# Performance work log

Hardware: AMD Instinct MI355X
Metric: run time of the kernel (lower is better)

The kernel has to match this reference:

```python
import jax, jax.numpy as jnp
import numpy as np

B, S, D = 2, 2048, 2048
E, F, TOP_K = 16, 768, 2
NORM_TOPK_PROB = True


def setup_inputs() -> dict:
    key = jax.random.key(0)
    ks = jax.random.split(key, 5)
    sc = 0.02
    return {
        "hidden_states": jax.random.normal(ks[0], (B, S, D), jnp.float32),
        "router_w": jax.random.normal(ks[1], (E, D), jnp.float32) * sc,
        "gate_w": jax.random.normal(ks[2], (E, F, D), jnp.float32) * sc,
        "up_w": jax.random.normal(ks[3], (E, F, D), jnp.float32) * sc,
        "down_w": jax.random.normal(ks[4], (E, D, F), jnp.float32) * sc,
    }


def reference(hidden_states, router_w, gate_w, up_w, down_w):
    b, s, d = hidden_states.shape
    x = hidden_states.reshape(-1, d)                      # [T, D]
    T = x.shape[0]
    # Router: logits, softmax in fp32, top-k
    router_logits = x @ router_w.T                        # [T, E]
    probs = jax.nn.softmax(router_logits.astype(jnp.float32), axis=-1)
    topk_w, topk_idx = jax.lax.top_k(probs, TOP_K)        # [T, K]
    if NORM_TOPK_PROB:
        topk_w = topk_w / jnp.sum(topk_w, axis=-1, keepdims=True)
    topk_w = topk_w.astype(x.dtype)
    # Combine weights as a dense [T, E] matrix (0 for unselected experts);
    # math-equivalent to the per-expert gather/index_add in the original.
    combine = jnp.zeros((T, E), x.dtype).at[jnp.arange(T)[:, None], topk_idx].add(topk_w)
    # Per-expert SwiGLU MLP on all tokens (zero-weight tokens contribute nothing)
    g = jax.nn.silu(jnp.einsum('td,efd->etf', x, gate_w))  # [E, T, F]
    u = jnp.einsum('td,efd->etf', x, up_w)                 # [E, T, F]
    h = (g * u) * combine.T[:, :, None]                    # weight before down-proj
    out = jnp.einsum('etf,edf->td', h, down_w)             # [T, D]
    return out.reshape(b, s, d), router_logits
```

## Files before the change

### kernel.cpp

```cpp
#include <hip/hip_runtime.h>
#include <stdint.h>


#define NTOK 4096
#define DIM  2048
#define NEXP 16
#define FDIM 768
#define BK   32

#define WS_CNT     0
#define WS_CUR     256
#define WS_NTILES  512
#define WS_TILE_E  576
#define WS_TILE_B  736
#define WS_TOKE    1024
#define WS_TOKW    9216
#define WS_SLOTT   17408
#define SLOTW_NEW  27648
#define SLOTW_OLD  26624
#define MAX_TILES  144

#define TMN 128
#define TNA 64
#define TNB 128
#define MAX_SLOTS_N 10240
#define MAX_TILES_N 80
#define TMO 64
#define MAX_SLOTS_O 9216

#define B_XBF  262144ull
#define B_H    (B_XBF + (size_t)NTOK*DIM*2)
#define B_GBF  (B_H + (size_t)MAX_SLOTS_N*FDIM*2)
#define B_UBF  (B_GBF + (size_t)NEXP*FDIM*DIM*2)
#define B_DBF  (B_UBF + (size_t)NEXP*FDIM*DIM*2)
#define WS_NEED (B_DBF + (size_t)NEXP*FDIM*DIM*2)
#define B_HOLD 143360ull

typedef __attribute__((ext_vector_type(8))) short short8;
typedef __attribute__((ext_vector_type(4))) float f32x4;

__device__ __forceinline__ unsigned short f2bf(float f) {
    unsigned u = __float_as_uint(f);
    return (unsigned short)((u + 0x7FFFu + ((u >> 16) & 1u)) >> 16);
}

__device__ __forceinline__ short8 cvt8(float4 v0, float4 v1) {
    short8 s;
    s[0] = (short)f2bf(v0.x); s[1] = (short)f2bf(v0.y);
    s[2] = (short)f2bf(v0.z); s[3] = (short)f2bf(v0.w);
    s[4] = (short)f2bf(v1.x); s[5] = (short)f2bf(v1.y);
    s[6] = (short)f2bf(v1.z); s[7] = (short)f2bf(v1.w);
    return s;
}

__device__ __forceinline__ void gl_lds16(const void* g, void* l) {
    __builtin_amdgcn_global_load_lds(
        (const __attribute__((address_space(1))) unsigned int*)g,
        (__attribute__((address_space(3))) unsigned int*)l, 16, 0, 0);
}

__global__ __launch_bounds__(256) void cvt_k(const float* __restrict__ s,
                                             unsigned short* __restrict__ d, int n8) {
    int i = blockIdx.x * 256 + threadIdx.x;
    if (i < n8) {
        const float4* p = (const float4*)(s + (size_t)i * 8);
        *(short8*)(d + (size_t)i * 8) = cvt8(p[0], p[1]);
    }
}

__global__ __launch_bounds__(256) void router_k(
    const float* __restrict__ x, const float* __restrict__ rw,
    float* __restrict__ logits_out, int* __restrict__ wsi, float* __restrict__ wsf)
{
    int wid = threadIdx.x >> 6, lane = threadIdx.x & 63;
    int t = blockIdx.x * 4 + wid;
    const float* xr = x + (size_t)t * DIM;

    float acc[NEXP];
#pragma unroll
    for (int e = 0; e < NEXP; e++) acc[e] = 0.f;
    for (int i = 0; i < DIM / 64; i++) {
        float xv = xr[i * 64 + lane];
#pragma unroll
        for (int e = 0; e < NEXP; e++) acc[e] += xv * rw[e * DIM + i * 64 + lane];
    }
#pragma unroll
    for (int e = 0; e < NEXP; e++) {
        float v = acc[e];
        for (int off = 32; off; off >>= 1) v += __shfl_down(v, off);
        acc[e] = v;
    }
    if (lane == 0) {
#pragma unroll
        for (int e = 0; e < NEXP; e++) logits_out[t * NEXP + e] = acc[e];
        int i0 = 0; float m0 = acc[0];
#pragma unroll
        for (int e = 1; e < NEXP; e++) if (acc[e] > m0) { m0 = acc[e]; i0 = e; }
        int i1 = -1; float m1 = -3.4e38f;
#pragma unroll
        for (int e = 0; e < NEXP; e++) if (e != i0 && acc[e] > m1) { m1 = acc[e]; i1 = e; }
        float w0 = 1.f / (1.f + __expf(m1 - m0));
        wsi[WS_TOKE + t * 2 + 0] = i0;
        wsi[WS_TOKE + t * 2 + 1] = i1;
        wsf[WS_TOKW + t * 2 + 0] = w0;
        wsf[WS_TOKW + t * 2 + 1] = 1.f - w0;
        atomicAdd(&wsi[WS_CNT + i0 * 16], 1);
        atomicAdd(&wsi[WS_CNT + i1 * 16], 1);
    }
}

__global__ void scan_k(int* __restrict__ wsi, float* __restrict__ wsf,
                       int tm, int slotw, int max_slots)
{
    if (threadIdx.x == 0) {
        int total = 0, tiles = 0;
        for (int e = 0; e < NEXP; e++) {
            int c = wsi[WS_CNT + e * 16];
            int nt = (c + tm - 1) / tm;
            wsi[WS_CNT + e * 16] = total;
            for (int j = 0; j < nt; j++) {
                wsi[WS_TILE_E + tiles] = e;
                wsi[WS_TILE_B + tiles] = total + j * tm;
                tiles++;
            }
            total += nt * tm;
        }
        wsi[WS_NTILES] = tiles;
    }
    for (int s = threadIdx.x; s < max_slots; s += blockDim.x) {
        wsi[WS_SLOTT + s] = 0;
        wsf[slotw + s] = 0.f;
    }
}

__global__ __launch_bounds__(256) void scatter_k(int* __restrict__ wsi,
                                                 float* __restrict__ wsf, int slotw)
{
    int t = blockIdx.x * blockDim.x + threadIdx.x;
    if (t >= NTOK) return;
#pragma unroll
    for (int k = 0; k < 2; k++) {
        int e = wsi[WS_TOKE + t * 2 + k];
        float w = wsf[WS_TOKW + t * 2 + k];
        int pos = atomicAdd(&wsi[WS_CUR + e * 16], 1);
        int s = wsi[WS_CNT + e * 16] + pos;
        wsi[WS_SLOTT + s] = t;
        wsf[slotw + s] = w;
    }
}


__global__ __launch_bounds__(256) void expertA_k(
    const unsigned short* __restrict__ xbf,
    const unsigned short* __restrict__ gbf,
    const unsigned short* __restrict__ ubf,
    const int* __restrict__ wsi, const float* __restrict__ wsf,
    unsigned short* __restrict__ H)
{
    __shared__ unsigned short As[TMN * BK];
    __shared__ unsigned short Gs[TNA * BK];
    __shared__ unsigned short Us[TNA * BK];
    __shared__ unsigned short Hs[TMN][TNA + 8];
    __shared__ int   Ts[TMN];
    __shared__ float Wl[TMN];

    int tile = blockIdx.y;
    if (tile >= wsi[WS_NTILES]) return;
    int e     = wsi[WS_TILE_E + tile];
    int slot0 = wsi[WS_TILE_B + tile];
    int f0    = blockIdx.x * TNA;
    int tid   = threadIdx.x;

    if (tid < TMN) {
        Ts[tid] = wsi[WS_SLOTT + slot0 + tid];
        Wl[tid] = wsf[SLOTW_NEW + slot0 + tid];
    }
    __syncthreads();

    int r0 = tid >> 2, seg = tid & 3;
    const unsigned short* ap0 = xbf + (size_t)Ts[r0] * DIM + seg * 8;
    const unsigned short* ap1 = xbf + (size_t)Ts[64 + r0] * DIM + seg * 8;
    const unsigned short* gp  = gbf + ((size_t)e * FDIM + f0 + r0) * DIM + seg * 8;
    const unsigned short* up  = ubf + ((size_t)e * FDIM + f0 + r0) * DIM + seg * 8;
    unsigned short* lA0 = &As[(size_t)tid * 8];
    unsigned short* lA1 = &As[(size_t)(256 + tid) * 8];
    unsigned short* lG  = &Gs[(size_t)tid * 8];
    unsigned short* lU  = &Us[(size_t)tid * 8];

    int wid = tid >> 6, lane = tid & 63;
    int wm = (wid >> 1) * 64, wn = (wid & 1) * 32;
    int lr = lane & 15, lk = (lane >> 4) * 8;

    f32x4 accg[4][2], accu[4][2];
#pragma unroll
    for (int i = 0; i < 4; i++)
#pragma unroll
        for (int j = 0; j < 2; j++) { accg[i][j] = (f32x4)0.f; accu[i][j] = (f32x4)0.f; }

    for (int k0 = 0; k0 < DIM; k0 += BK) {
        gl_lds16(ap0 + k0, lA0);
        gl_lds16(ap1 + k0, lA1);
        gl_lds16(gp + k0, lG);
        gl_lds16(up + k0, lU);
        __syncthreads();

        short8 a[4], g[2], u[2];
#pragma unroll
        for (int mi = 0; mi < 4; mi++)
            a[mi] = *(const short8*)&As[(wm + mi * 16 + lr) * BK + lk];
#pragma unroll
        for (int nj = 0; nj < 2; nj++) {
            g[nj] = *(const short8*)&Gs[(wn + nj * 16 + lr) * BK + lk];
            u[nj] = *(const short8*)&Us[(wn + nj * 16 + lr) * BK + lk];
        }
#pragma unroll
        for (int mi = 0; mi < 4; mi++)
#pragma unroll
            for (int nj = 0; nj < 2; nj++) {
                accg[mi][nj] = __builtin_amdgcn_mfma_f32_16x16x32_bf16(a[mi], g[nj], accg[mi][nj], 0, 0, 0);
                accu[mi][nj] = __builtin_amdgcn_mfma_f32_16x16x32_bf16(a[mi], u[nj], accu[mi][nj], 0, 0, 0);
            }
        __syncthreads();
    }

#pragma unroll
    for (int mi = 0; mi < 4; mi++)
#pragma unroll
        for (int nj = 0; nj < 2; nj++)
#pragma unroll
            for (int r = 0; r < 4; r++) {
                int m = wm + mi * 16 + (lane >> 4) * 4 + r;
                int n = wn + nj * 16 + lr;
                float g = accg[mi][nj][r];
                float u = accu[mi][nj][r];
                float sg = g / (1.f + __expf(-g));
                Hs[m][n] = f2bf(sg * u * Wl[m]);
            }
    __syncthreads();

    int row = tid >> 1, cb = (tid & 1) * 32;
    unsigned short* dst = H + (size_t)(slot0 + row) * FDIM + f0 + cb;
#pragma unroll
    for (int c = 0; c < 4; c++)
        *(short8*)(dst + c * 8) = *(const short8*)&Hs[row][cb + c * 8];
}

__global__ __launch_bounds__(256) void expertB_k(
    const unsigned short* __restrict__ H, const unsigned short* __restrict__ dbf,
    const int* __restrict__ wsi, float* __restrict__ out)
{
    __shared__ unsigned short As[TMN * BK];
    __shared__ unsigned short Bs[TNB * BK];
    __shared__ int Ts[TMN];

    int tile = blockIdx.y;
    if (tile >= wsi[WS_NTILES]) return;
    int e     = wsi[WS_TILE_E + tile];
    int slot0 = wsi[WS_TILE_B + tile];
    int d0    = blockIdx.x * TNB;
    int tid   = threadIdx.x;

    if (tid < TMN) Ts[tid] = wsi[WS_SLOTT + slot0 + tid];
    __syncthreads();

    int r0 = tid >> 2, seg = tid & 3;
    const unsigned short* ap0 = H + (size_t)(slot0 + r0) * FDIM + seg * 8;
    const unsigned short* ap1 = H + (size_t)(slot0 + 64 + r0) * FDIM + seg * 8;
    const unsigned short* bp0 = dbf + ((size_t)e * DIM + d0 + r0) * FDIM + seg * 8;
    const unsigned short* bp1 = dbf + ((size_t)e * DIM + d0 + 64 + r0) * FDIM + seg * 8;
    unsigned short* lA0 = &As[(size_t)tid * 8];
    unsigned short* lA1 = &As[(size_t)(256 + tid) * 8];
    unsigned short* lB0 = &Bs[(size_t)tid * 8];
    unsigned short* lB1 = &Bs[(size_t)(256 + tid) * 8];

    int wid = tid >> 6, lane = tid & 63;
    int wm = (wid >> 1) * 64, wn = (wid & 1) * 64;
    int lr = lane & 15, lk = (lane >> 4) * 8;

    f32x4 acc[4][4];
#pragma unroll
    for (int i = 0; i < 4; i++)
#pragma unroll
        for (int j = 0; j < 4; j++) acc[i][j] = (f32x4)0.f;

    for (int k0 = 0; k0 < FDIM; k0 += BK) {
        gl_lds16(ap0 + k0, lA0);
        gl_lds16(ap1 + k0, lA1);
        gl_lds16(bp0 + k0, lB0);
        gl_lds16(bp1 + k0, lB1);
        __syncthreads();

        short8 a[4], b[4];
#pragma unroll
        for (int i = 0; i < 4; i++) {
            a[i] = *(const short8*)&As[(wm + i * 16 + lr) * BK + lk];
            b[i] = *(const short8*)&Bs[(wn + i * 16 + lr) * BK + lk];
        }
#pragma unroll
        for (int mi = 0; mi < 4; mi++)
#pragma unroll
            for (int nj = 0; nj < 4; nj++)
                acc[mi][nj] = __builtin_amdgcn_mfma_f32_16x16x32_bf16(a[mi], b[nj], acc[mi][nj], 0, 0, 0);
        __syncthreads();
    }

#pragma unroll
    for (int mi = 0; mi < 4; mi++)
#pragma unroll
        for (int nj = 0; nj < 4; nj++)
#pragma unroll
            for (int r = 0; r < 4; r++) {
                int m = wm + mi * 16 + (lane >> 4) * 4 + r;
                int n = d0 + wn + nj * 16 + lr;
                atomicAdd(&out[(size_t)Ts[m] * DIM + n], acc[mi][nj][r]);
            }
}


__global__ __launch_bounds__(256) void expertA64_k(
    const float* __restrict__ x, const float* __restrict__ gw, const float* __restrict__ uw,
    const int* __restrict__ wsi, const float* __restrict__ wsf,
    unsigned short* __restrict__ H)
{
    __shared__ unsigned short As[TMO][40];
    __shared__ unsigned short Bg[TMO][40];
    __shared__ unsigned short Bu[TMO][40];
    __shared__ unsigned short Hs[TMO][72];
    __shared__ int   Ts[TMO];
    __shared__ float Wl[TMO];

    int tile = blockIdx.y;
    if (tile >= wsi[WS_NTILES]) return;
    int e     = wsi[WS_TILE_E + tile];
    int slot0 = wsi[WS_TILE_B + tile];
    int f0    = blockIdx.x * 64;
    int tid   = threadIdx.x;

    if (tid < TMO) {
        Ts[tid] = wsi[WS_SLOTT + slot0 + tid];
        Wl[tid] = wsf[SLOTW_OLD + slot0 + tid];
    }
    __syncthreads();

    int row = tid >> 2, seg = tid & 3;
    const float* aRow = x  + (size_t)Ts[row] * DIM + seg * 8;
    const float* gRow = gw + ((size_t)e * FDIM + f0 + row) * DIM + seg * 8;
    const float* uRow = uw + ((size_t)e * FDIM + f0 + row) * DIM + seg * 8;

    int wid = tid >> 6, lane = tid & 63;
    int wm = (wid >> 1) * 32, wn = (wid & 1) * 32;
    int lr = lane & 15, lk = (lane >> 4) * 8;

    f32x4 accg[2][2], accu[2][2];
#pragma unroll
    for (int i = 0; i < 2; i++)
#pragma unroll
        for (int j = 0; j < 2; j++) { accg[i][j] = (f32x4)0.f; accu[i][j] = (f32x4)0.f; }

    for (int k0 = 0; k0 < DIM; k0 += BK) {
        { const float4* p = (const float4*)(aRow + k0); *(short8*)&As[row][seg * 8] = cvt8(p[0], p[1]); }
        { const float4* p = (const float4*)(gRow + k0); *(short8*)&Bg[row][seg * 8] = cvt8(p[0], p[1]); }
        { const float4* p = (const float4*)(uRow + k0); *(short8*)&Bu[row][seg * 8] = cvt8(p[0], p[1]); }
        __syncthreads();
        short8 a0 = *(const short8*)&As[wm + lr][lk];
        short8 a1 = *(const short8*)&As[wm + 16 + lr][lk];
        short8 g0 = *(const short8*)&Bg[wn + lr][lk];
        short8 g1 = *(const short8*)&Bg[wn + 16 + lr][lk];
        short8 u0 = *(const short8*)&Bu[wn + lr][lk];
        short8 u1 = *(const short8*)&Bu[wn + 16 + lr][lk];
        accg[0][0] = __builtin_amdgcn_mfma_f32_16x16x32_bf16(a0, g0, accg[0][0], 0, 0, 0);
        accg[0][1] = __builtin_amdgcn_mfma_f32_16x16x32_bf16(a0, g1, accg[0][1], 0, 0, 0);
        accg[1][0] = __builtin_amdgcn_mfma_f32_16x16x32_bf16(a1, g0, accg[1][0], 0, 0, 0);
        accg[1][1] = __builtin_amdgcn_mfma_f32_16x16x32_bf16(a1, g1, accg[1][1], 0, 0, 0);
        accu[0][0] = __builtin_amdgcn_mfma_f32_16x16x32_bf16(a0, u0, accu[0][0], 0, 0, 0);
        accu[0][1] = __builtin_amdgcn_mfma_f32_16x16x32_bf16(a0, u1, accu[0][1], 0, 0, 0);
        accu[1][0] = __builtin_amdgcn_mfma_f32_16x16x32_bf16(a1, u0, accu[1][0], 0, 0, 0);
        accu[1][1] = __builtin_amdgcn_mfma_f32_16x16x32_bf16(a1, u1, accu[1][1], 0, 0, 0);
        __syncthreads();
    }
#pragma unroll
    for (int mi = 0; mi < 2; mi++)
#pragma unroll
        for (int ni = 0; ni < 2; ni++)
#pragma unroll
            for (int r = 0; r < 4; r++) {
                int m = wm + mi * 16 + (lane >> 4) * 4 + r;
                int n = wn + ni * 16 + lr;
                float g = accg[mi][ni][r];
                float u = accu[mi][ni][r];
                Hs[m][n] = f2bf((g / (1.f + __expf(-g))) * u * Wl[m]);
            }
    __syncthreads();
    unsigned short* dst = H + (size_t)(slot0 + row) * FDIM + f0 + seg * 16;
    *(short8*)dst       = *(const short8*)&Hs[row][seg * 16];
    *(short8*)(dst + 8) = *(const short8*)&Hs[row][seg * 16 + 8];
}

__global__ __launch_bounds__(256) void expertB64_k(
    const unsigned short* __restrict__ H, const float* __restrict__ dw,
    const int* __restrict__ wsi, float* __restrict__ out)
{
    __shared__ unsigned short As[TMO][40];
    __shared__ unsigned short Bd[TMO][40];
    __shared__ int Ts[TMO];

    int tile = blockIdx.y;
    if (tile >= wsi[WS_NTILES]) return;
    int e     = wsi[WS_TILE_E + tile];
    int slot0 = wsi[WS_TILE_B + tile];
    int d0    = blockIdx.x * 64;
    int tid   = threadIdx.x;

    if (tid < TMO) Ts[tid] = wsi[WS_SLOTT + slot0 + tid];
    __syncthreads();

    int row = tid >> 2, seg = tid & 3;
    const unsigned short* aRow = H + (size_t)(slot0 + row) * FDIM + seg * 8;
    const float* dRow = dw + ((size_t)e * DIM + d0 + row) * FDIM + seg * 8;

    int wid = tid >> 6, lane = tid & 63;
    int wm = (wid >> 1) * 32, wn = (wid & 1) * 32;
    int lr = lane & 15, lk = (lane >> 4) * 8;

    f32x4 acc[2][2];
#pragma unroll
    for (int i = 0; i < 2; i++)
#pragma unroll
        for (int j = 0; j < 2; j++) acc[i][j] = (f32x4)0.f;

    for (int k0 = 0; k0 < FDIM; k0 += BK) {
        *(short8*)&As[row][seg * 8] = *(const short8*)(aRow + k0);
        { const float4* p = (const float4*)(dRow + k0); *(short8*)&Bd[row][seg * 8] = cvt8(p[0], p[1]); }
        __syncthreads();
        short8 a0 = *(const short8*)&As[wm + lr][lk];
        short8 a1 = *(const short8*)&As[wm + 16 + lr][lk];
        short8 b0 = *(const short8*)&Bd[wn + lr][lk];
        short8 b1 = *(const short8*)&Bd[wn + 16 + lr][lk];
        acc[0][0] = __builtin_amdgcn_mfma_f32_16x16x32_bf16(a0, b0, acc[0][0], 0, 0, 0);
        acc[0][1] = __builtin_amdgcn_mfma_f32_16x16x32_bf16(a0, b1, acc[0][1], 0, 0, 0);
        acc[1][0] = __builtin_amdgcn_mfma_f32_16x16x32_bf16(a1, b0, acc[1][0], 0, 0, 0);
        acc[1][1] = __builtin_amdgcn_mfma_f32_16x16x32_bf16(a1, b1, acc[1][1], 0, 0, 0);
        __syncthreads();
    }
#pragma unroll
    for (int mi = 0; mi < 2; mi++)
#pragma unroll
        for (int ni = 0; ni < 2; ni++)
#pragma unroll
            for (int r = 0; r < 4; r++) {
                int m = wm + mi * 16 + (lane >> 4) * 4 + r;
                int n = d0 + wn + ni * 16 + lr;
                atomicAdd(&out[(size_t)Ts[m] * DIM + n], acc[mi][ni][r]);
            }
}

extern "C" void kernel_launch(void* const* d_in, const int* in_sizes, int n_in,
                              void* d_out, int out_size, void* d_ws, size_t ws_size,
                              hipStream_t stream) {
    const float* x  = (const float*)d_in[0];
    const float* rw = (const float*)d_in[1];
    const float* gw = (const float*)d_in[2];
    const float* uw = (const float*)d_in[3];
    const float* dw = (const float*)d_in[4];
    float* out    = (float*)d_out;
    float* logits = out + (size_t)NTOK * DIM;
    int*   wsi = (int*)d_ws;
    float* wsf = (float*)d_ws;

    hipMemsetAsync(d_out, 0, (size_t)NTOK * DIM * sizeof(float), stream);
    hipMemsetAsync(d_ws, 0, 4096, stream);

    router_k<<<NTOK / 4, 256, 0, stream>>>(x, rw, logits, wsi, wsf);

    if (ws_size >= WS_NEED) {
        unsigned short* xbf = (unsigned short*)((char*)d_ws + B_XBF);
        unsigned short* H   = (unsigned short*)((char*)d_ws + B_H);
        unsigned short* gbf = (unsigned short*)((char*)d_ws + B_GBF);
        unsigned short* ubf = (unsigned short*)((char*)d_ws + B_UBF);
        unsigned short* dbf = (unsigned short*)((char*)d_ws + B_DBF);
        const int nw8 = NEXP * FDIM * DIM / 8;
        cvt_k<<<NTOK * DIM / 8 / 256, 256, 0, stream>>>(x, xbf, NTOK * DIM / 8);
        cvt_k<<<nw8 / 256, 256, 0, stream>>>(gw, gbf, nw8);
        cvt_k<<<nw8 / 256, 256, 0, stream>>>(uw, ubf, nw8);
        cvt_k<<<nw8 / 256, 256, 0, stream>>>(dw, dbf, nw8);
        scan_k   <<<1, 256, 0, stream>>>(wsi, wsf, TMN, SLOTW_NEW, MAX_SLOTS_N);
        scatter_k<<<NTOK / 256, 256, 0, stream>>>(wsi, wsf, SLOTW_NEW);
        expertA_k<<<dim3(FDIM / TNA, MAX_TILES_N), 256, 0, stream>>>(xbf, gbf, ubf, wsi, wsf, H);
        expertB_k<<<dim3(DIM / TNB, MAX_TILES_N), 256, 0, stream>>>(H, dbf, wsi, out);
    } else {
        unsigned short* H = (unsigned short*)((char*)d_ws + B_HOLD);
        scan_k   <<<1, 256, 0, stream>>>(wsi, wsf, TMO, SLOTW_OLD, MAX_SLOTS_O);
        scatter_k<<<NTOK / 256, 256, 0, stream>>>(wsi, wsf, SLOTW_OLD);
        expertA64_k<<<dim3(FDIM / 64, MAX_TILES), 256, 0, stream>>>(x, gw, uw, wsi, wsf, H);
        expertB64_k<<<dim3(DIM / 64, MAX_TILES), 256, 0, stream>>>(H, dw, wsi, out);
    }
}
```

Measured before the change: 660.5 us.

## Double-buffer expert GEMMs, replace atomic scatter with slot output plus combine

expertB now writes per-slot fp32 results into a workspace buffer (reusing the gate/up bf16 region) instead of doing atomicAdd into the output. A new combine_k kernel sums each token's two slots, which also removes the full-output memset. expertA and expertB gain double-buffered LDS staging so the next k-tile loads while the current one computes. The x-to-bf16 conversion is folded into the router, and the three weight conversions are merged into one launch. The trade-off is extra global traffic for the slot buffer and more LDS per block.

```diff
diff --git a/kernel.cpp b/kernel.cpp
--- a/kernel.cpp
+++ b/kernel.cpp
@@ -18,6 +18,7 @@
 #define WS_SLOTT   17408
 #define SLOTW_NEW  27648
 #define SLOTW_OLD  26624
+#define WS_TOKSLOT 40960
 #define MAX_TILES  144
 
 #define TMN 128
@@ -34,6 +35,7 @@
 #define B_UBF  (B_GBF + (size_t)NEXP*FDIM*DIM*2)
 #define B_DBF  (B_UBF + (size_t)NEXP*FDIM*DIM*2)
 #define WS_NEED (B_DBF + (size_t)NEXP*FDIM*DIM*2)
+#define B_OSL  B_GBF
 #define B_HOLD 143360ull
 
 typedef __attribute__((ext_vector_type(8))) short short8;
@@ -59,18 +61,26 @@
         (__attribute__((address_space(3))) unsigned int*)l, 16, 0, 0);
 }
 
-__global__ __launch_bounds__(256) void cvt_k(const float* __restrict__ s,
-                                             unsigned short* __restrict__ d, int n8) {
+__global__ __launch_bounds__(256) void cvtw_k(
+    const float* __restrict__ g, const float* __restrict__ u, const float* __restrict__ d,
+    unsigned short* __restrict__ go, unsigned short* __restrict__ uo,
+    unsigned short* __restrict__ dd, int n8)
+{
     int i = blockIdx.x * 256 + threadIdx.x;
-    if (i < n8) {
-        const float4* p = (const float4*)(s + (size_t)i * 8);
-        *(short8*)(d + (size_t)i * 8) = cvt8(p[0], p[1]);
-    }
+    if (i >= n8) return;
+    const float* s;
+    unsigned short* o;
+    if (blockIdx.y == 0)      { s = g; o = go; }
+    else if (blockIdx.y == 1) { s = u; o = uo; }
+    else                      { s = d; o = dd; }
+    const float4* p = (const float4*)(s + (size_t)i * 8);
+    *(short8*)(o + (size_t)i * 8) = cvt8(p[0], p[1]);
 }
 
 __global__ __launch_bounds__(256) void router_k(
     const float* __restrict__ x, const float* __restrict__ rw,
-    float* __restrict__ logits_out, int* __restrict__ wsi, float* __restrict__ wsf)
+    float* __restrict__ logits_out, int* __restrict__ wsi, float* __restrict__ wsf,
+    unsigned short* __restrict__ xbf)
 {
     int wid = threadIdx.x >> 6, lane = threadIdx.x & 63;
     int t = blockIdx.x * 4 + wid;
@@ -81,6 +91,7 @@
     for (int e = 0; e < NEXP; e++) acc[e] = 0.f;
     for (int i = 0; i < DIM / 64; i++) {
         float xv = xr[i * 64 + lane];
+        if (xbf) xbf[(size_t)t * DIM + i * 64 + lane] = f2bf(xv);
 #pragma unroll
         for (int e = 0; e < NEXP; e++) acc[e] += xv * rw[e * DIM + i * 64 + lane];
     }
@@ -146,6 +157,7 @@
         int s = wsi[WS_CNT + e * 16] + pos;
         wsi[WS_SLOTT + s] = t;
         wsf[slotw + s] = w;
+        wsi[WS_TOKSLOT + t * 2 + k] = s;
     }
 }
 
@@ -157,10 +169,14 @@
     const int* __restrict__ wsi, const float* __restrict__ wsf,
     unsigned short* __restrict__ H)
 {
-    __shared__ unsigned short As[TMN * BK];
-    __shared__ unsigned short Gs[TNA * BK];
-    __shared__ unsigned short Us[TNA * BK];
-    __shared__ unsigned short Hs[TMN][TNA + 8];
+    __shared__ union {
+        struct {
+            unsigned short A[2][TMN * BK];
+            unsigned short G[2][TNA * BK];
+            unsigned short U[2][TNA * BK];
+        } st;
+        unsigned short Hs[TMN][TNA + 8];
+    } sh;
     __shared__ int   Ts[TMN];
     __shared__ float Wl[TMN];
 
@@ -182,10 +198,6 @@
     const unsigned short* ap1 = xbf + (size_t)Ts[64 + r0] * DIM + seg * 8;
     const unsigned short* gp  = gbf + ((size_t)e * FDIM + f0 + r0) * DIM + seg * 8;
     const unsigned short* up  = ubf + ((size_t)e * FDIM + f0 + r0) * DIM + seg * 8;
-    unsigned short* lA0 = &As[(size_t)tid * 8];
-    unsigned short* lA1 = &As[(size_t)(256 + tid) * 8];
-    unsigned short* lG  = &Gs[(size_t)tid * 8];
-    unsigned short* lU  = &Us[(size_t)tid * 8];
 
     int wid = tid >> 6, lane = tid & 63;
     int wm = (wid >> 1) * 64, wn = (wid & 1) * 32;
@@ -197,21 +209,21 @@
 #pragma unroll
         for (int j = 0; j < 2; j++) { accg[i][j] = (f32x4)0.f; accu[i][j] = (f32x4)0.f; }
 
-    for (int k0 = 0; k0 < DIM; k0 += BK) {
-        gl_lds16(ap0 + k0, lA0);
-        gl_lds16(ap1 + k0, lA1);
-        gl_lds16(gp + k0, lG);
-        gl_lds16(up + k0, lU);
-        __syncthreads();
-
+    auto stage = [&](int b, int k0) {
+        gl_lds16(ap0 + k0, &sh.st.A[b][(size_t)tid * 8]);
+        gl_lds16(ap1 + k0, &sh.st.A[b][(size_t)(256 + tid) * 8]);
+        gl_lds16(gp + k0,  &sh.st.G[b][(size_t)tid * 8]);
+        gl_lds16(up + k0,  &sh.st.U[b][(size_t)tid * 8]);
+    };
+    auto comp = [&](int b) {
         short8 a[4], g[2], u[2];
 #pragma unroll
         for (int mi = 0; mi < 4; mi++)
-            a[mi] = *(const short8*)&As[(wm + mi * 16 + lr) * BK + lk];
+            a[mi] = *(const short8*)&sh.st.A[b][(wm + mi * 16 + lr) * BK + lk];
 #pragma unroll
         for (int nj = 0; nj < 2; nj++) {
-            g[nj] = *(const short8*)&Gs[(wn + nj * 16 + lr) * BK + lk];
-            u[nj] = *(const short8*)&Us[(wn + nj * 16 + lr) * BK + lk];
+            g[nj] = *(const short8*)&sh.st.G[b][(wn + nj * 16 + lr) * BK + lk];
+            u[nj] = *(const short8*)&sh.st.U[b][(wn + nj * 16 + lr) * BK + lk];
         }
 #pragma unroll
         for (int mi = 0; mi < 4; mi++)
@@ -220,6 +232,16 @@
                 accg[mi][nj] = __builtin_amdgcn_mfma_f32_16x16x32_bf16(a[mi], g[nj], accg[mi][nj], 0, 0, 0);
                 accu[mi][nj] = __builtin_amdgcn_mfma_f32_16x16x32_bf16(a[mi], u[nj], accu[mi][nj], 0, 0, 0);
             }
+    };
+
+    stage(0, 0);
+    __syncthreads();
+    for (int k0 = 0; k0 < DIM; k0 += 2 * BK) {
+        if (k0 + BK < DIM) stage(1, k0 + BK);
+        comp(0);
+        __syncthreads();
+        if (k0 + 2 * BK < DIM) stage(0, k0 + 2 * BK);
+        comp(1);
         __syncthreads();
     }
 
@@ -234,7 +256,7 @@
                 float g = accg[mi][nj][r];
                 float u = accu[mi][nj][r];
                 float sg = g / (1.f + __expf(-g));
-                Hs[m][n] = f2bf(sg * u * Wl[m]);
+                sh.Hs[m][n] = f2bf(sg * u * Wl[m]);
             }
     __syncthreads();
 
@@ -242,16 +264,15 @@
     unsigned short* dst = H + (size_t)(slot0 + row) * FDIM + f0 + cb;
 #pragma unroll
     for (int c = 0; c < 4; c++)
-        *(short8*)(dst + c * 8) = *(const short8*)&Hs[row][cb + c * 8];
+        *(short8*)(dst + c * 8) = *(const short8*)&sh.Hs[row][cb + c * 8];
 }
 
 __global__ __launch_bounds__(256) void expertB_k(
     const unsigned short* __restrict__ H, const unsigned short* __restrict__ dbf,
-    const int* __restrict__ wsi, float* __restrict__ out)
-{
-    __shared__ unsigned short As[TMN * BK];
-    __shared__ unsigned short Bs[TNB * BK];
-    __shared__ int Ts[TMN];
+    const int* __restrict__ wsi, float* __restrict__ O)
+{
+    __shared__ unsigned short As[2][TMN * BK];
+    __shared__ unsigned short Bs[2][TNB * BK];
 
     int tile = blockIdx.y;
     if (tile >= wsi[WS_NTILES]) return;
@@ -260,18 +281,11 @@
     int d0    = blockIdx.x * TNB;
     int tid   = threadIdx.x;
 
-    if (tid < TMN) Ts[tid] = wsi[WS_SLOTT + slot0 + tid];
-    __syncthreads();
-
     int r0 = tid >> 2, seg = tid & 3;
     const unsigned short* ap0 = H + (size_t)(slot0 + r0) * FDIM + seg * 8;
     const unsigned short* ap1 = H + (size_t)(slot0 + 64 + r0) * FDIM + seg * 8;
     const unsigned short* bp0 = dbf + ((size_t)e * DIM + d0 + r0) * FDIM + seg * 8;
     const unsigned short* bp1 = dbf + ((size_t)e * DIM + d0 + 64 + r0) * FDIM + seg * 8;
-    unsigned short* lA0 = &As[(size_t)tid * 8];
-    unsigned short* lA1 = &As[(size_t)(256 + tid) * 8];
-    unsigned short* lB0 = &Bs[(size_t)tid * 8];
-    unsigned short* lB1 = &Bs[(size_t)(256 + tid) * 8];
 
     int wid = tid >> 6, lane = tid & 63;
     int wm = (wid >> 1) * 64, wn = (wid & 1) * 64;
@@ -283,24 +297,34 @@
 #pragma unroll
         for (int j = 0; j < 4; j++) acc[i][j] = (f32x4)0.f;
 
-    for (int k0 = 0; k0 < FDIM; k0 += BK) {
-        gl_lds16(ap0 + k0, lA0);
-        gl_lds16(ap1 + k0, lA1);
-        gl_lds16(bp0 + k0, lB0);
-        gl_lds16(bp1 + k0, lB1);
-        __syncthreads();
-
+    auto stage = [&](int b, int k0) {
+        gl_lds16(ap0 + k0, &As[b][(size_t)tid * 8]);
+        gl_lds16(ap1 + k0, &As[b][(size_t)(256 + tid) * 8]);
+        gl_lds16(bp0 + k0, &Bs[b][(size_t)tid * 8]);
+        gl_lds16(bp1 + k0, &Bs[b][(size_t)(256 + tid) * 8]);
+    };
+    auto comp = [&](int bb) {
         short8 a[4], b[4];
 #pragma unroll
         for (int i = 0; i < 4; i++) {
-            a[i] = *(const short8*)&As[(wm + i * 16 + lr) * BK + lk];
-            b[i] = *(const short8*)&Bs[(wn + i * 16 + lr) * BK + lk];
+            a[i] = *(const short8*)&As[bb][(wm + i * 16 + lr) * BK + lk];
+            b[i] = *(const short8*)&Bs[bb][(wn + i * 16 + lr) * BK + lk];
         }
 #pragma unroll
         for (int mi = 0; mi < 4; mi++)
 #pragma unroll
             for (int nj = 0; nj < 4; nj++)
                 acc[mi][nj] = __builtin_amdgcn_mfma_f32_16x16x32_bf16(a[mi], b[nj], acc[mi][nj], 0, 0, 0);
+    };
+
+    stage(0, 0);
+    __syncthreads();
+    for (int k0 = 0; k0 < FDIM; k0 += 2 * BK) {
+        if (k0 + BK < FDIM) stage(1, k0 + BK);
+        comp(0);
+        __syncthreads();
+        if (k0 + 2 * BK < FDIM) stage(0, k0 + 2 * BK);
+        comp(1);
         __syncthreads();
     }
 
@@ -312,8 +336,22 @@
             for (int r = 0; r < 4; r++) {
                 int m = wm + mi * 16 + (lane >> 4) * 4 + r;
                 int n = d0 + wn + nj * 16 + lr;
-                atomicAdd(&out[(size_t)Ts[m] * DIM + n], acc[mi][nj][r]);
+                O[(size_t)(slot0 + m) * DIM + n] = acc[mi][nj][r];
             }
+}
+
+__global__ __launch_bounds__(256) void combine_k(
+    const float* __restrict__ O, const int* __restrict__ wsi, float* __restrict__ out)
+{
+    int i = blockIdx.x * 256 + threadIdx.x;
+    int t = i >> 9, c = i & 511;
+    int s0 = wsi[WS_TOKSLOT + t * 2 + 0];
+    int s1 = wsi[WS_TOKSLOT + t * 2 + 1];
+    float4 a = *((const float4*)(O + (size_t)s0 * DIM) + c);
+    float4 b = *((const float4*)(O + (size_t)s1 * DIM) + c);
+    float4 r;
+    r.x = a.x + b.x; r.y = a.y + b.y; r.z = a.z + b.z; r.w = a.w + b.w;
+    *((float4*)(out + (size_t)t * DIM) + c) = r;
 }
 
 
@@ -467,10 +505,7 @@
     int*   wsi = (int*)d_ws;
     float* wsf = (float*)d_ws;
 
-    hipMemsetAsync(d_out, 0, (size_t)NTOK * DIM * sizeof(float), stream);
     hipMemsetAsync(d_ws, 0, 4096, stream);
-
-    router_k<<<NTOK / 4, 256, 0, stream>>>(x, rw, logits, wsi, wsf);
 
     if (ws_size >= WS_NEED) {
         unsigned short* xbf = (unsigned short*)((char*)d_ws + B_XBF);
@@ -478,17 +513,19 @@
         unsigned short* gbf = (unsigned short*)((char*)d_ws + B_GBF);
         unsigned short* ubf = (unsigned short*)((char*)d_ws + B_UBF);
         unsigned short* dbf = (unsigned short*)((char*)d_ws + B_DBF);
+        float*          Osl = (float*)((char*)d_ws + B_OSL);
         const int nw8 = NEXP * FDIM * DIM / 8;
-        cvt_k<<<NTOK * DIM / 8 / 256, 256, 0, stream>>>(x, xbf, NTOK * DIM / 8);
-        cvt_k<<<nw8 / 256, 256, 0, stream>>>(gw, gbf, nw8);
-        cvt_k<<<nw8 / 256, 256, 0, stream>>>(uw, ubf, nw8);
-        cvt_k<<<nw8 / 256, 256, 0, stream>>>(dw, dbf, nw8);
+        router_k<<<NTOK / 4, 256, 0, stream>>>(x, rw, logits, wsi, wsf, xbf);
+        cvtw_k<<<dim3(nw8 / 256, 3), 256, 0, stream>>>(gw, uw, dw, gbf, ubf, dbf, nw8);
         scan_k   <<<1, 256, 0, stream>>>(wsi, wsf, TMN, SLOTW_NEW, MAX_SLOTS_N);
         scatter_k<<<NTOK / 256, 256, 0, stream>>>(wsi, wsf, SLOTW_NEW);
         expertA_k<<<dim3(FDIM / TNA, MAX_TILES_N), 256, 0, stream>>>(xbf, gbf, ubf, wsi, wsf, H);
-        expertB_k<<<dim3(DIM / TNB, MAX_TILES_N), 256, 0, stream>>>(H, dbf, wsi, out);
+        expertB_k<<<dim3(DIM / TNB, MAX_TILES_N), 256, 0, stream>>>(H, dbf, wsi, Osl);
+        combine_k<<<NTOK * DIM / 4 / 256, 256, 0, stream>>>(Osl, wsi, out);
     } else {
         unsigned short* H = (unsigned short*)((char*)d_ws + B_HOLD);
+        hipMemsetAsync(d_out, 0, (size_t)NTOK * DIM * sizeof(float), stream);
+        router_k<<<NTOK / 4, 256, 0, stream>>>(x, rw, logits, wsi, wsf, nullptr);
         scan_k   <<<1, 256, 0, stream>>>(wsi, wsf, TMO, SLOTW_OLD, MAX_SLOTS_O);
         scatter_k<<<NTOK / 256, 256, 0, stream>>>(wsi, wsf, SLOTW_OLD);
         expertA64_k<<<dim3(FDIM / 64, MAX_TILES), 256, 0, stream>>>(x, gw, uw, wsi, wsf, H);
```

New measurement: 581.2 us. -12.0%, faster.
